# Optimization experiments

Measured on AMD Instinct MI355X. Metric: run time of the kernel, lower is better.

## Reference

```python
import jax, jax.numpy as jnp
import numpy as np

DIM = 128
WS = 7          # window size
NH = 4          # num heads
N = WS * WS     # tokens per window = 49
GRID = 56       # 224/4 token grid -> 8x8 = 64 windows per image
NUM_WIN = (GRID // WS) ** 2  # 64
IMG_B = 64
SCALE = (DIM // NH) ** -0.5


def _relative_position_index():
    coords = np.stack(np.meshgrid(np.arange(WS), np.arange(WS), indexing='ij'))  # (2,WS,WS)
    flat = coords.reshape(2, -1)                         # (2, N)
    rel = flat[:, :, None] - flat[:, None, :]            # (2, N, N)
    rel = rel.transpose(1, 2, 0).astype(np.int32)        # (N, N, 2)
    rel[:, :, 0] += WS - 1
    rel[:, :, 1] += WS - 1
    rel[:, :, 0] *= 2 * WS - 1
    return jnp.asarray(rel.sum(-1))                      # (N, N) int32


def _shift_mask():
    # Swin shifted-window attention mask: shift = WS // 2, off-group pairs get -100.
    shift = WS // 2
    img = np.zeros((GRID, GRID), dtype=np.int32)
    cnt = 0
    segs = (slice(0, -WS), slice(-WS, -shift), slice(-shift, None))
    for hs in segs:
        for ws_ in segs:
            img[hs, ws_] = cnt
            cnt += 1
    # window partition -> (NUM_WIN, N)
    w = img.reshape(GRID // WS, WS, GRID // WS, WS).transpose(0, 2, 1, 3).reshape(NUM_WIN, N)
    diff = w[:, :, None] - w[:, None, :]
    return jnp.asarray(np.where(diff != 0, -100.0, 0.0).astype(np.float32))  # (NUM_WIN, N, N)


def setup_inputs() -> dict:
    key = jax.random.key(0)
    ks = jax.random.split(key, 6)
    B = IMG_B * NUM_WIN  # 4096
    x = jax.random.normal(ks[0], (B, N, DIM), dtype=jnp.float32)
    qkv_w = jax.random.normal(ks[1], (3 * DIM, DIM), dtype=jnp.float32) * (DIM ** -0.5)
    qkv_b = jnp.zeros((3 * DIM,), dtype=jnp.float32)
    proj_w = jax.random.normal(ks[2], (DIM, DIM), dtype=jnp.float32) * (DIM ** -0.5)
    proj_b = jnp.zeros((DIM,), dtype=jnp.float32)
    rel_bias_table = jax.random.normal(ks[3], ((2 * WS - 1) ** 2, NH), dtype=jnp.float32) * 0.02
    return {
        'x': x,
        'mask': _shift_mask(),
        'qkv_w': qkv_w,
        'qkv_b': qkv_b,
        'proj_w': proj_w,
        'proj_b': proj_b,
        'rel_bias_table': rel_bias_table,
        'rel_index': _relative_position_index(),
    }


def reference(x, mask, qkv_w, qkv_b, proj_w, proj_b, rel_bias_table, rel_index):
    B, n, C = x.shape
    hd = C // NH
    qkv = (x @ qkv_w.T + qkv_b).reshape(B, n, 3, NH, hd)
    q = qkv[:, :, 0].transpose(0, 2, 1, 3) * SCALE   # (B, H, N, hd)
    k = qkv[:, :, 1].transpose(0, 2, 1, 3)
    v = qkv[:, :, 2].transpose(0, 2, 1, 3)
    attn = jnp.einsum('bhnd,bhmd->bhnm', q, k)       # (B, H, N, N)
    bias = rel_bias_table[rel_index.reshape(-1)].reshape(n, n, NH).transpose(2, 0, 1)
    attn = attn + bias[None]
    nW = mask.shape[0]
    attn = attn.reshape(B // nW, nW, NH, n, n) + mask[None, :, None]
    attn = jax.nn.softmax(attn.reshape(B, NH, n, n), axis=-1)
    out = jnp.einsum('bhnm,bhmd->bhnd', attn, v).transpose(0, 2, 1, 3).reshape(B, n, C)
    return out @ proj_w.T + proj_b
```

## Files before the change

kernel.cpp:

```cpp
#include <hip/hip_runtime.h>


#define NTOK  49
#define DIMC  128
#define NBLK  4096
#define SCALE 0.17677669529663687f

typedef __attribute__((ext_vector_type(8))) short bf16x8;
typedef __attribute__((ext_vector_type(4))) float f32x4;

#define WS_QKVW 0
#define WS_PROJW 49152
#define WS_BIAS  65536
#define WS_TOTAL 81920

#define XS_OFF 0
#define XS_STRIDE 136
#define PS_OFF 6664
#define PS_STRIDE 72
#define QS_OFF 10192
#define QS_STRIDE 40
#define KS_OFF 20432
#define VT_OFF 30672
#define VT_STRIDE 72
#define SMEM_TOT 39888

__device__ __forceinline__ unsigned short f2b(float f) {
    union { float f; unsigned int i; } v; v.f = f;
    unsigned int r = (v.i + 0x7FFFu + ((v.i >> 16) & 1u)) >> 16;
    return (unsigned short)r;
}
__device__ __forceinline__ float b2f_lo(unsigned int u) {
    union { unsigned int i; float f; } v; v.i = u << 16; return v.f;
}
__device__ __forceinline__ float b2f_hi(unsigned int u) {
    union { unsigned int i; float f; } v; v.i = u & 0xFFFF0000u; return v.f;
}

__device__ __forceinline__ int seg3(int c) { return (c < 49) ? 0 : ((c < 53) ? 1 : 2); }

__global__ __launch_bounds__(256)
void prep(const float* __restrict__ qkv_w, const float* __restrict__ proj_w,
          const float* __restrict__ bias_t, const int* __restrict__ rel_idx,
          unsigned short* __restrict__ ws)
{
    int idx = blockIdx.x * 256 + threadIdx.x;
    if (idx < 49152) {
        ws[WS_QKVW + idx] = f2b(qkv_w[idx]);
    } else if (idx < 65536) {
        ws[idx] = f2b(proj_w[idx - 49152]);
    } else if (idx < 81920) {
        int i = idx - 65536;
        int reg = i & 3, lane = (i >> 2) & 63, nt = (i >> 8) & 3,
            mt = (i >> 10) & 3, h = (i >> 12) & 3;
        int row = mt * 16 + (lane >> 4) * 4 + reg;
        int col = nt * 16 + (lane & 15);
        float v = 0.f;
        if (row < NTOK && col < NTOK)
            v = bias_t[rel_idx[row * NTOK + col] * 4 + h];
        ws[idx] = f2b(v);
    }
}

__global__ __launch_bounds__(256, 2)
void win_attn(const float* __restrict__ x,
              const float* __restrict__ qkv_b,
              const float* __restrict__ proj_b,
              const unsigned short* __restrict__ ws,
              float* __restrict__ out)
{
    __shared__ unsigned short smem[SMEM_TOT];
    const int b    = blockIdx.x;
    const int w    = b & 63;
    const int tid  = threadIdx.x;
    const int wv   = tid >> 6;
    const int lane = tid & 63;
    const int qg   = lane >> 4;
    const int l15  = lane & 15;

    {
        const float4* xg = (const float4*)(x + (size_t)b * (NTOK * DIMC));
        for (int i = tid; i < NTOK * DIMC / 4; i += 256) {
            float4 v = xg[i];
            int row = i >> 5, col = (i & 31) * 4;
            ushort4 st = { f2b(v.x), f2b(v.y), f2b(v.z), f2b(v.w) };
            *(ushort4*)(smem + XS_OFF + row * XS_STRIDE + col) = st;
        }
    }
    __syncthreads();

    {
        const unsigned short* qw = ws + WS_QKVW;
        #pragma unroll
        for (int part = 0; part < 3; part++) {
            #pragma unroll
            for (int half = 0; half < 2; half++) {
                const int jt = part * 8 + wv * 2 + half;
                const int j  = jt * 16 + l15;
                bf16x8 bf[4];
                #pragma unroll
                for (int ks_ = 0; ks_ < 4; ks_++)
                    bf[ks_] = *(const bf16x8*)(qw + j * DIMC + ks_ * 32 + qg * 8);
                const float bias = qkv_b[j];
                #pragma unroll
                for (int mt = 0; mt < 4; mt++) {
                    f32x4 acc = { bias, bias, bias, bias };
                    int ar = mt * 16 + l15; if (ar > 48) ar = 48;
                    #pragma unroll
                    for (int ks_ = 0; ks_ < 4; ks_++) {
                        bf16x8 af = *(const bf16x8*)(smem + XS_OFF + ar * XS_STRIDE + ks_ * 32 + qg * 8);
                        acc = __builtin_amdgcn_mfma_f32_16x16x32_bf16(af, bf[ks_], acc, 0, 0, 0);
                    }
                    const int d = half * 16 + l15;
                    if (part == 0) {
                        #pragma unroll
                        for (int r = 0; r < 4; r++) {
                            int row = mt * 16 + qg * 4 + r;
                            smem[QS_OFF + (wv * 64 + row) * QS_STRIDE + d] = f2b(acc[r] * SCALE);
                        }
                    } else if (part == 1) {
                        #pragma unroll
                        for (int r = 0; r < 4; r++) {
                            int row = mt * 16 + qg * 4 + r;
                            smem[KS_OFF + (wv * 64 + row) * QS_STRIDE + d] = f2b(acc[r]);
                        }
                    } else {
                        ushort4 st = { f2b(acc[0]), f2b(acc[1]), f2b(acc[2]), f2b(acc[3]) };
                        *(ushort4*)(smem + VT_OFF + (wv * 32 + d) * VT_STRIDE + mt * 16 + qg * 4) = st;
                    }
                }
            }
        }
    }
    __syncthreads();

    const int wy = w >> 3, wx = w & 7;
    int g_row[4], g_col[4]; bool vcol[4];
    #pragma unroll
    for (int r = 0; r < 4; r++) {
        int t = wv * 16 + qg * 4 + r;
        int ty = (t * 9363) >> 16, tx = t - ty * 7;
        int y = wy * 7 + ty, xx = wx * 7 + tx;
        g_row[r] = seg3(y) * 3 + seg3(xx);
    }
    #pragma unroll
    for (int nt = 0; nt < 4; nt++) {
        int t = nt * 16 + l15;
        int ty = (t * 9363) >> 16, tx = t - ty * 7;
        int y = wy * 7 + ty, xx = wx * 7 + tx;
        g_col[nt] = seg3(y) * 3 + seg3(xx);
        vcol[nt] = t < NTOK;
    }

    const int r0 = wv * 16;
    for (int h = 0; h < 4; h++) {
        bf16x8 aq = *(const bf16x8*)(smem + QS_OFF + (h * 64 + r0 + l15) * QS_STRIDE + qg * 8);
        float s[4][4];
        #pragma unroll
        for (int nt = 0; nt < 4; nt++) {
            bf16x8 bk = *(const bf16x8*)(smem + KS_OFF + (h * 64 + nt * 16 + l15) * QS_STRIDE + qg * 8);
            f32x4 z = { 0.f, 0.f, 0.f, 0.f };
            f32x4 c = __builtin_amdgcn_mfma_f32_16x16x32_bf16(aq, bk, z, 0, 0, 0);
            uint2 bb = *(const uint2*)(ws + WS_BIAS + (((h * 4 + wv) * 4 + nt) * 64 + lane) * 4);
            float bv[4] = { b2f_lo(bb.x), b2f_hi(bb.x), b2f_lo(bb.y), b2f_hi(bb.y) };
            #pragma unroll
            for (int r = 0; r < 4; r++) {
                float v = c[r] + bv[r];
                v += (g_row[r] == g_col[nt]) ? 0.f : -100.f;
                s[nt][r] = vcol[nt] ? v : -1e30f;
            }
        }
        float p[4][4];
        #pragma unroll
        for (int r = 0; r < 4; r++) {
            float mx = fmaxf(fmaxf(s[0][r], s[1][r]), fmaxf(s[2][r], s[3][r]));
            mx = fmaxf(mx, __shfl_xor(mx, 1));
            mx = fmaxf(mx, __shfl_xor(mx, 2));
            mx = fmaxf(mx, __shfl_xor(mx, 4));
            mx = fmaxf(mx, __shfl_xor(mx, 8));
            float sum = 0.f;
            #pragma unroll
            for (int nt = 0; nt < 4; nt++) {
                float e = vcol[nt] ? __expf(s[nt][r] - mx) : 0.f;
                p[nt][r] = e; sum += e;
            }
            sum += __shfl_xor(sum, 1);
            sum += __shfl_xor(sum, 2);
            sum += __shfl_xor(sum, 4);
            sum += __shfl_xor(sum, 8);
            float inv = 1.f / sum;
            #pragma unroll
            for (int nt = 0; nt < 4; nt++) p[nt][r] *= inv;
        }
        #pragma unroll
        for (int nt = 0; nt < 4; nt++)
            #pragma unroll
            for (int r = 0; r < 4; r++) {
                int row = r0 + qg * 4 + r;
                if (row < NTOK)
                    smem[PS_OFF + row * PS_STRIDE + nt * 16 + l15] = f2b(p[nt][r]);
            }
        int ar = r0 + l15; if (ar > 48) ar = 48;
        #pragma unroll
        for (int nt2 = 0; nt2 < 2; nt2++) {
            f32x4 acc = { 0.f, 0.f, 0.f, 0.f };
            #pragma unroll
            for (int ks2 = 0; ks2 < 2; ks2++) {
                bf16x8 ap = *(const bf16x8*)(smem + PS_OFF + ar * PS_STRIDE + ks2 * 32 + qg * 8);
                bf16x8 bv = *(const bf16x8*)(smem + VT_OFF + (h * 32 + nt2 * 16 + l15) * VT_STRIDE + ks2 * 32 + qg * 8);
                acc = __builtin_amdgcn_mfma_f32_16x16x32_bf16(ap, bv, acc, 0, 0, 0);
            }
            #pragma unroll
            for (int r = 0; r < 4; r++) {
                int row = r0 + qg * 4 + r;
                if (row < NTOK)
                    smem[XS_OFF + row * XS_STRIDE + h * 32 + nt2 * 16 + l15] = f2b(acc[r]);
            }
        }
    }
    __syncthreads();

    {
        const unsigned short* pw = ws + WS_PROJW;
        float* ob = out + (size_t)b * (NTOK * DIMC);
        #pragma unroll
        for (int half = 0; half < 2; half++) {
            const int jt = wv * 2 + half;
            const int j  = jt * 16 + l15;
            bf16x8 bf[4];
            #pragma unroll
            for (int ks_ = 0; ks_ < 4; ks_++)
                bf[ks_] = *(const bf16x8*)(pw + j * DIMC + ks_ * 32 + qg * 8);
            const float pb = proj_b[j];
            #pragma unroll
            for (int mt = 0; mt < 4; mt++) {
                f32x4 acc = { pb, pb, pb, pb };
                int ar = mt * 16 + l15; if (ar > 48) ar = 48;
                #pragma unroll
                for (int ks_ = 0; ks_ < 4; ks_++) {
                    bf16x8 af = *(const bf16x8*)(smem + XS_OFF + ar * XS_STRIDE + ks_ * 32 + qg * 8);
                    acc = __builtin_amdgcn_mfma_f32_16x16x32_bf16(af, bf[ks_], acc, 0, 0, 0);
                }
                #pragma unroll
                for (int r = 0; r < 4; r++) {
                    int row = mt * 16 + qg * 4 + r;
                    if (row < NTOK) ob[row * DIMC + j] = acc[r];
                }
            }
        }
    }
}

extern "C" void kernel_launch(void* const* d_in, const int* in_sizes, int n_in,
                              void* d_out, int out_size, void* d_ws, size_t ws_size,
                              hipStream_t stream) {
    const float* x      = (const float*)d_in[0];
    const float* qkv_w  = (const float*)d_in[2];
    const float* qkv_b  = (const float*)d_in[3];
    const float* proj_w = (const float*)d_in[4];
    const float* proj_b = (const float*)d_in[5];
    const float* bias_t = (const float*)d_in[6];
    const int*   relidx = (const int*)d_in[7];
    float*       outp   = (float*)d_out;
    unsigned short* ws  = (unsigned short*)d_ws;

    prep<<<WS_TOTAL / 256, 256, 0, stream>>>(qkv_w, proj_w, bias_t, relidx, ws);
    win_attn<<<NBLK, 256, 0, stream>>>(x, qkv_b, proj_b, ws, outp);
}
```

Baseline: 307.1 us.

## Hoist x fragments into registers, cheapen bf16 conversion, fold Q scale into weights

Measured after the change: 299.0 us. 1.03x faster.

```diff
diff --git a/kernel.cpp b/kernel.cpp
--- a/kernel.cpp
+++ b/kernel.cpp
@@ -25,10 +25,13 @@
 #define VT_STRIDE 72
 #define SMEM_TOT 39888
 
-__device__ __forceinline__ unsigned short f2b(float f) {
+__device__ __forceinline__ unsigned int pkbf2(float f0, float f1) {
+    union { float f; unsigned int i; } a, b; a.f = f0; b.f = f1;
+    return __builtin_amdgcn_perm(b.i + 0x8000u, a.i + 0x8000u, 0x07060302u);
+}
+__device__ __forceinline__ unsigned short f2b_r(float f) {
     union { float f; unsigned int i; } v; v.f = f;
-    unsigned int r = (v.i + 0x7FFFu + ((v.i >> 16) & 1u)) >> 16;
-    return (unsigned short)r;
+    return (unsigned short)((v.i + 0x8000u) >> 16);
 }
 __device__ __forceinline__ float b2f_lo(unsigned int u) {
     union { unsigned int i; float f; } v; v.i = u << 16; return v.f;
@@ -45,12 +48,20 @@
           unsigned short* __restrict__ ws)
 {
     int idx = blockIdx.x * 256 + threadIdx.x;
-    if (idx < 49152) {
-        ws[WS_QKVW + idx] = f2b(qkv_w[idx]);
-    } else if (idx < 65536) {
-        ws[idx] = f2b(proj_w[idx - 49152]);
-    } else if (idx < 81920) {
-        int i = idx - 65536;
+    if (idx < 8192) {
+        int base = idx * 8;
+        const float* sp = (base < 49152) ? (qkv_w + base) : (proj_w + (base - 49152));
+        float sc = (base < 16384) ? SCALE : 1.0f;
+        float4 a = *(const float4*)sp;
+        float4 b = *(const float4*)(sp + 4);
+        uint4 u;
+        u.x = pkbf2(a.x * sc, a.y * sc);
+        u.y = pkbf2(a.z * sc, a.w * sc);
+        u.z = pkbf2(b.x * sc, b.y * sc);
+        u.w = pkbf2(b.z * sc, b.w * sc);
+        *(uint4*)(ws + base) = u;
+    } else {
+        int i = idx - 8192;
         int reg = i & 3, lane = (i >> 2) & 63, nt = (i >> 8) & 3,
             mt = (i >> 10) & 3, h = (i >> 12) & 3;
         int row = mt * 16 + (lane >> 4) * 4 + reg;
@@ -58,7 +69,7 @@
         float v = 0.f;
         if (row < NTOK && col < NTOK)
             v = bias_t[rel_idx[row * NTOK + col] * 4 + h];
-        ws[idx] = f2b(v);
+        ws[WS_BIAS + i] = f2b_r(v);
     }
 }
 
@@ -83,11 +94,20 @@
         for (int i = tid; i < NTOK * DIMC / 4; i += 256) {
             float4 v = xg[i];
             int row = i >> 5, col = (i & 31) * 4;
-            ushort4 st = { f2b(v.x), f2b(v.y), f2b(v.z), f2b(v.w) };
-            *(ushort4*)(smem + XS_OFF + row * XS_STRIDE + col) = st;
+            uint2 u; u.x = pkbf2(v.x, v.y); u.y = pkbf2(v.z, v.w);
+            *(uint2*)(smem + XS_OFF + row * XS_STRIDE + col) = u;
         }
     }
     __syncthreads();
+
+    bf16x8 af[4][4];
+    #pragma unroll
+    for (int mt = 0; mt < 4; mt++) {
+        int ar = mt * 16 + l15; if (ar > 48) ar = 48;
+        #pragma unroll
+        for (int ks_ = 0; ks_ < 4; ks_++)
+            af[mt][ks_] = *(const bf16x8*)(smem + XS_OFF + ar * XS_STRIDE + ks_ * 32 + qg * 8);
+    }
 
     {
         const unsigned short* qw = ws + WS_QKVW;
@@ -101,32 +121,29 @@
                 #pragma unroll
                 for (int ks_ = 0; ks_ < 4; ks_++)
                     bf[ks_] = *(const bf16x8*)(qw + j * DIMC + ks_ * 32 + qg * 8);
-                const float bias = qkv_b[j];
+                const float bias = (part == 0) ? qkv_b[j] * SCALE : qkv_b[j];
                 #pragma unroll
                 for (int mt = 0; mt < 4; mt++) {
                     f32x4 acc = { bias, bias, bias, bias };
-                    int ar = mt * 16 + l15; if (ar > 48) ar = 48;
                     #pragma unroll
-                    for (int ks_ = 0; ks_ < 4; ks_++) {
-                        bf16x8 af = *(const bf16x8*)(smem + XS_OFF + ar * XS_STRIDE + ks_ * 32 + qg * 8);
-                        acc = __builtin_amdgcn_mfma_f32_16x16x32_bf16(af, bf[ks_], acc, 0, 0, 0);
-                    }
+                    for (int ks_ = 0; ks_ < 4; ks_++)
+                        acc = __builtin_amdgcn_mfma_f32_16x16x32_bf16(af[mt][ks_], bf[ks_], acc, 0, 0, 0);
                     const int d = half * 16 + l15;
                     if (part == 0) {
                         #pragma unroll
                         for (int r = 0; r < 4; r++) {
                             int row = mt * 16 + qg * 4 + r;
-                            smem[QS_OFF + (wv * 64 + row) * QS_STRIDE + d] = f2b(acc[r] * SCALE);
+                            smem[QS_OFF + (wv * 64 + row) * QS_STRIDE + d] = f2b_r(acc[r]);
                         }
                     } else if (part == 1) {
                         #pragma unroll
                         for (int r = 0; r < 4; r++) {
                             int row = mt * 16 + qg * 4 + r;
-                            smem[KS_OFF + (wv * 64 + row) * QS_STRIDE + d] = f2b(acc[r]);
+                            smem[KS_OFF + (wv * 64 + row) * QS_STRIDE + d] = f2b_r(acc[r]);
                         }
                     } else {
-                        ushort4 st = { f2b(acc[0]), f2b(acc[1]), f2b(acc[2]), f2b(acc[3]) };
-                        *(ushort4*)(smem + VT_OFF + (wv * 32 + d) * VT_STRIDE + mt * 16 + qg * 4) = st;
+                        uint2 u; u.x = pkbf2(acc[0], acc[1]); u.y = pkbf2(acc[2], acc[3]);
+                        *(uint2*)(smem + VT_OFF + (wv * 32 + d) * VT_STRIDE + mt * 16 + qg * 4) = u;
                     }
                 }
             }
@@ -140,15 +157,13 @@
     for (int r = 0; r < 4; r++) {
         int t = wv * 16 + qg * 4 + r;
         int ty = (t * 9363) >> 16, tx = t - ty * 7;
-        int y = wy * 7 + ty, xx = wx * 7 + tx;
-        g_row[r] = seg3(y) * 3 + seg3(xx);
+        g_row[r] = seg3(wy * 7 + ty) * 3 + seg3(wx * 7 + tx);
     }
     #pragma unroll
     for (int nt = 0; nt < 4; nt++) {
         int t = nt * 16 + l15;
         int ty = (t * 9363) >> 16, tx = t - ty * 7;
-        int y = wy * 7 + ty, xx = wx * 7 + tx;
-        g_col[nt] = seg3(y) * 3 + seg3(xx);
+        g_col[nt] = seg3(wy * 7 + ty) * 3 + seg3(wx * 7 + tx);
         vcol[nt] = t < NTOK;
     }
 
@@ -198,35 +213,43 @@
             for (int r = 0; r < 4; r++) {
                 int row = r0 + qg * 4 + r;
                 if (row < NTOK)
-                    smem[PS_OFF + row * PS_STRIDE + nt * 16 + l15] = f2b(p[nt][r]);
-            }
-        int ar = r0 + l15; if (ar > 48) ar = 48;
-        #pragma unroll
-        for (int nt2 = 0; nt2 < 2; nt2++) {
-            f32x4 acc = { 0.f, 0.f, 0.f, 0.f };
-            #pragma unroll
-            for (int ks2 = 0; ks2 < 2; ks2++) {
-                bf16x8 ap = *(const bf16x8*)(smem + PS_OFF + ar * PS_STRIDE + ks2 * 32 + qg * 8);
+                    smem[PS_OFF + row * PS_STRIDE + nt * 16 + l15] = f2b_r(p[nt][r]);
+            }
+        int ar2 = r0 + l15; if (ar2 > 48) ar2 = 48;
+        f32x4 accO[2] = { { 0.f, 0.f, 0.f, 0.f }, { 0.f, 0.f, 0.f, 0.f } };
+        #pragma unroll
+        for (int ks2 = 0; ks2 < 2; ks2++) {
+            bf16x8 ap = *(const bf16x8*)(smem + PS_OFF + ar2 * PS_STRIDE + ks2 * 32 + qg * 8);
+            #pragma unroll
+            for (int nt2 = 0; nt2 < 2; nt2++) {
                 bf16x8 bv = *(const bf16x8*)(smem + VT_OFF + (h * 32 + nt2 * 16 + l15) * VT_STRIDE + ks2 * 32 + qg * 8);
-                acc = __builtin_amdgcn_mfma_f32_16x16x32_bf16(ap, bv, acc, 0, 0, 0);
-            }
+                accO[nt2] = __builtin_amdgcn_mfma_f32_16x16x32_bf16(ap, bv, accO[nt2], 0, 0, 0);
+            }
+        }
+        #pragma unroll
+        for (int nt2 = 0; nt2 < 2; nt2++)
             #pragma unroll
             for (int r = 0; r < 4; r++) {
                 int row = r0 + qg * 4 + r;
                 if (row < NTOK)
-                    smem[XS_OFF + row * XS_STRIDE + h * 32 + nt2 * 16 + l15] = f2b(acc[r]);
-            }
-        }
+                    smem[XS_OFF + row * XS_STRIDE + h * 32 + nt2 * 16 + l15] = f2b_r(accO[nt2][r]);
+            }
     }
     __syncthreads();
 
     {
+        #pragma unroll
+        for (int mt = 0; mt < 4; mt++) {
+            int ar = mt * 16 + l15; if (ar > 48) ar = 48;
+            #pragma unroll
+            for (int ks_ = 0; ks_ < 4; ks_++)
+                af[mt][ks_] = *(const bf16x8*)(smem + XS_OFF + ar * XS_STRIDE + ks_ * 32 + qg * 8);
+        }
         const unsigned short* pw = ws + WS_PROJW;
         float* ob = out + (size_t)b * (NTOK * DIMC);
         #pragma unroll
         for (int half = 0; half < 2; half++) {
-            const int jt = wv * 2 + half;
-            const int j  = jt * 16 + l15;
+            const int j = (wv * 2 + half) * 16 + l15;
             bf16x8 bf[4];
             #pragma unroll
             for (int ks_ = 0; ks_ < 4; ks_++)
@@ -235,12 +258,9 @@
             #pragma unroll
             for (int mt = 0; mt < 4; mt++) {
                 f32x4 acc = { pb, pb, pb, pb };
-                int ar = mt * 16 + l15; if (ar > 48) ar = 48;
-                #pragma unroll
-                for (int ks_ = 0; ks_ < 4; ks_++) {
-                    bf16x8 af = *(const bf16x8*)(smem + XS_OFF + ar * XS_STRIDE + ks_ * 32 + qg * 8);
-                    acc = __builtin_amdgcn_mfma_f32_16x16x32_bf16(af, bf[ks_], acc, 0, 0, 0);
-                }
+                #pragma unroll
+                for (int ks_ = 0; ks_ < 4; ks_++)
+                    acc = __builtin_amdgcn_mfma_f32_16x16x32_bf16(af[mt][ks_], bf[ks_], acc, 0, 0, 0);
                 #pragma unroll
                 for (int r = 0; r < 4; r++) {
                     int row = mt * 16 + qg * 4 + r;
@@ -264,6 +284,6 @@
     float*       outp   = (float*)d_out;
     unsigned short* ws  = (unsigned short*)d_ws;
 
-    prep<<<WS_TOTAL / 256, 256, 0, stream>>>(qkv_w, proj_w, bias_t, relidx, ws);
+    prep<<<96, 256, 0, stream>>>(qkv_w, proj_w, bias_t, relidx, ws);
     win_attn<<<NBLK, 256, 0, stream>>>(x, qkv_b, proj_b, ws, outp);
 }
```
